# Kernel tuning notes

Measured on AMD Instinct MI355X. Metric: run time of the kernel, lower is better.

Reference implementation:

```python
import jax, jax.numpy as jnp
from jax import lax
import numpy as np

B, T, D, H = 32, 2048, 512, 512


def setup_inputs() -> dict:
    key = jax.random.key(0)
    k1, k2, k3, k4, k5 = jax.random.split(key, 5)
    s = 1.0 / np.sqrt(H)
    return {
        "inputs": jax.random.normal(k1, (B, T, D), dtype=jnp.float32),
        "h_prev": jax.random.normal(k2, (B, H), dtype=jnp.float32),
        # LSTMCell parameters, gate order (i, f, g, o) stacked along first dim
        "W_ih": jax.random.uniform(k3, (4 * H, D), jnp.float32, -s, s),
        "W_hh": jax.random.uniform(k4, (4 * H, H), jnp.float32, -s, s),
        "b": jax.random.uniform(k5, (4 * H,), jnp.float32, -s, s),
    }


def reference(inputs, h_prev, W_ih, W_hh, b):
    # inputs: [B, T, D], h_prev: [B, H]
    batch = inputs.shape[0]
    hid = h_prev.shape[1]
    c_prev = jnp.zeros((batch, hid), dtype=inputs.dtype)
    # Precompute input projections for all timesteps: [T, B, 4H]
    x_proj = jnp.einsum("btd,gd->tbg", inputs, W_ih) + b

    def step(carry, xp_t):
        h, c = carry
        gates = xp_t + h @ W_hh.T  # [B, 4H]
        i, f, g, o = jnp.split(gates, 4, axis=-1)
        i = jax.nn.sigmoid(i)
        f = jax.nn.sigmoid(f)
        g = jnp.tanh(g)
        o = jax.nn.sigmoid(o)
        c_next = f * c + i * g
        h_next = o * jnp.tanh(c_next)
        return (h_next, c_next), None

    (h_last, _), _ = lax.scan(step, (h_prev, c_prev), x_proj)
    return h_last
```

## Files before the change

kernel.cpp:

```cpp
#include <hip/hip_runtime.h>

typedef _Float16 f16;
typedef _Float16 f16x4 __attribute__((ext_vector_type(4)));
typedef _Float16 f16x8 __attribute__((ext_vector_type(8)));
typedef float f32x4 __attribute__((ext_vector_type(4)));
typedef unsigned long long u64;
typedef unsigned short u16;

#define NB 32
#define NT 2048
#define ND 512
#define NH 512
#define NWG 16
#define SENTW 0xFFFFFFFFFFFFFFFFull
#define SENTH ((u16)0xFFFFu)

__device__ __forceinline__ float sigf(float x)  { return 1.0f / (1.0f + __expf(-x)); }
__device__ __forceinline__ float tanhf_(float x){ return 2.0f / (1.0f + __expf(-2.0f * x)) - 1.0f; }

__device__ __forceinline__ bool has_sent(u64 x) {
  u64 a = x & (x >> 8); a &= (a >> 4); a &= (a >> 2); a &= (a >> 1);
  return (a & 0x0001000100010001ull) != 0ull;
}

__device__ __forceinline__ int lds_idx(int w) {
  const int m = w >> 7, c0 = (w & 127) << 2;
  const int kt = c0 >> 5, half = m >> 4;
  const int lane16 = (((c0 & 31) >> 3) << 4) + (m & 15);
  return ((kt * 2 + half) * 64 + lane16) * 8 + (c0 & 7);
}

__global__ void lstm_init(const float* __restrict__ hprev, u64* __restrict__ hg4) {
  const int g = blockIdx.x * 256 + threadIdx.x;
  const int m = g >> 7, c0 = (g & 127) << 2;
  const float* s = hprev + m * NH + c0;
  union { u64 u; f16 h[4]; } pk;
  pk.h[0] = (f16)s[0]; pk.h[1] = (f16)s[1]; pk.h[2] = (f16)s[2]; pk.h[3] = (f16)s[3];
  hg4[g] = pk.u;
  hg4[4096 + g] = SENTW;
  hg4[2 * 4096 + g] = SENTW;
  hg4[3 * 4096 + g] = SENTW;
}

__global__ void __launch_bounds__(256, 1)
lstm_xproj(const float* __restrict__ X, const float* __restrict__ Wih,
           const float* __restrict__ bias, f16* __restrict__ xp) {
  __shared__ f16 x_lds[16384];
  const int tid = threadIdx.x, lane = tid & 63;
  const int wv = tid >> 6, s = wv & 1, bt = wv >> 1;
  const int l15 = lane & 15, ko = (lane >> 4) * 8;
  const int cb = blockIdx.y, tb = blockIdx.x;
  const int colg = cb * 32 + s * 16 + l15;
  const int b0 = bt * 16 + (lane >> 4) * 4;

  f16x8 wf[4][16];
  float bs[4];
#pragma unroll
  for (int q = 0; q < 4; ++q) {
    const size_t grow = (size_t)(q * NH + colg);
    bs[q] = bias[grow];
#pragma unroll
    for (int kt = 0; kt < 16; ++kt) {
      const float* src = Wih + grow * ND + kt * 32 + ko;
      f32x4 u0 = *(const f32x4*)src, u1 = *(const f32x4*)(src + 4);
      f16x8 w;
      w[0]=(f16)u0[0]; w[1]=(f16)u0[1]; w[2]=(f16)u0[2]; w[3]=(f16)u0[3];
      w[4]=(f16)u1[0]; w[5]=(f16)u1[1]; w[6]=(f16)u1[2]; w[7]=(f16)u1[3];
      wf[q][kt] = w;
    }
  }

  for (int tt = 0; tt < 32; ++tt) {
    const int t = tb * 32 + tt;
#pragma unroll
    for (int i = 0; i < 16; ++i) {
      const int w = tid + 256 * i;
      const int m = w >> 7, c0 = (w & 127) << 2;
      f32x4 v = *(const f32x4*)(X + ((size_t)m * NT + t) * ND + c0);
      union { u64 u; f16 h[4]; } pk;
      pk.h[0]=(f16)v[0]; pk.h[1]=(f16)v[1]; pk.h[2]=(f16)v[2]; pk.h[3]=(f16)v[3];
      *(u64*)&x_lds[lds_idx(w)] = pk.u;
    }
    __syncthreads();

    f32x4 acc[4] = {{0,0,0,0},{0,0,0,0},{0,0,0,0},{0,0,0,0}};
#pragma unroll
    for (int kt = 0; kt < 16; ++kt) {
      f16x8 af = *(const f16x8*)&x_lds[((kt * 2 + bt) * 64 + lane) * 8];
      acc[0] = __builtin_amdgcn_mfma_f32_16x16x32_f16(af, wf[0][kt], acc[0], 0, 0, 0);
      acc[1] = __builtin_amdgcn_mfma_f32_16x16x32_f16(af, wf[1][kt], acc[1], 0, 0, 0);
      acc[2] = __builtin_amdgcn_mfma_f32_16x16x32_f16(af, wf[2][kt], acc[2], 0, 0, 0);
      acc[3] = __builtin_amdgcn_mfma_f32_16x16x32_f16(af, wf[3][kt], acc[3], 0, 0, 0);
    }
#pragma unroll
    for (int q = 0; q < 4; ++q) {
      f16x4 o;
      o[0]=(f16)(acc[q][0]+bs[q]); o[1]=(f16)(acc[q][1]+bs[q]);
      o[2]=(f16)(acc[q][2]+bs[q]); o[3]=(f16)(acc[q][3]+bs[q]);
      *(f16x4*)&xp[((((size_t)t * 4 + q) * 512) + colg) * 32 + b0] = o;
    }
    __syncthreads();
  }
}

__global__ void __launch_bounds__(256, 1)
lstm_rec(const float* __restrict__ Whh,
         const f16*   __restrict__ xp,
         float* __restrict__ out,
         u64* __restrict__ hg4) {
  __shared__ f16 h_lin[2][16384];

  const int tid  = threadIdx.x;
  const int wgid = blockIdx.x;
  const int lane = tid & 63;
  const int wv   = tid >> 6, s = wv & 1, bt = wv >> 1;
  const int l15  = lane & 15, ko = (lane >> 4) * 8;
  const int colg = wgid * 32 + s * 16 + l15;
  const int b0   = bt * 16 + (lane >> 4) * 4;

  f16x8 wf[4][16];
#pragma unroll
  for (int q = 0; q < 4; ++q) {
    const size_t grow = (size_t)(q * NH + colg);
#pragma unroll
    for (int kt = 0; kt < 16; ++kt) {
      const float* src = Whh + grow * NH + kt * 32 + ko;
      f32x4 u0 = *(const f32x4*)src, u1 = *(const f32x4*)(src + 4);
      f16x8 w;
      w[0]=(f16)u0[0]; w[1]=(f16)u0[1]; w[2]=(f16)u0[2]; w[3]=(f16)u0[3];
      w[4]=(f16)u1[0]; w[5]=(f16)u1[1]; w[6]=(f16)u1[2]; w[7]=(f16)u1[3];
      wf[q][kt] = w;
    }
  }

  u16* hgh = (u16*)hg4;

  f16x4 xpv[4];
#pragma unroll
  for (int q = 0; q < 4; ++q)
    xpv[q] = *(const f16x4*)&xp[(((size_t)0 * 4 + q) * 512 + colg) * 32 + b0];

  float c[4] = {0.f, 0.f, 0.f, 0.f};

  for (int t = 0; t < NT; ++t) {
    {
      u16* rb = hgh + (size_t)((t + 2) & 3) * 16384;
#pragma unroll
      for (int r = 0; r < 4; ++r)
        __hip_atomic_store(rb + (b0 + r) * 512 + colg, SENTH,
                           __ATOMIC_RELAXED, __HIP_MEMORY_SCOPE_AGENT);
    }
    const int tn = (t < NT - 1) ? t + 1 : NT - 1;
    f16x4 xpn[4];
#pragma unroll
    for (int q = 0; q < 4; ++q)
      xpn[q] = *(const f16x4*)&xp[(((size_t)tn * 4 + q) * 512 + colg) * 32 + b0];

    u64 hv16[16];
    {
      u64* src = hg4 + (size_t)(t & 3) * 4096;
#pragma unroll
      for (int i = 0; i < 16; ++i)
        hv16[i] = __hip_atomic_load(src + tid + 256 * i, __ATOMIC_RELAXED, __HIP_MEMORY_SCOPE_AGENT);
      while (true) {
        unsigned int bad = 0;
#pragma unroll
        for (int i = 0; i < 16; ++i) if (has_sent(hv16[i])) bad |= (1u << i);
        if (!__any(bad != 0)) break;
#pragma unroll
        for (int i = 0; i < 16; ++i)
          if (bad & (1u << i))
            hv16[i] = __hip_atomic_load(src + tid + 256 * i, __ATOMIC_RELAXED, __HIP_MEMORY_SCOPE_AGENT);
      }
    }
    asm volatile("s_waitcnt vmcnt(0)" ::: "memory");

    f16* hb = h_lin[t & 1];
#pragma unroll
    for (int i = 0; i < 16; ++i)
      *(u64*)&hb[lds_idx(tid + 256 * i)] = hv16[i];
    __syncthreads();

    f32x4 acc[4] = {{0,0,0,0},{0,0,0,0},{0,0,0,0},{0,0,0,0}};
#pragma unroll
    for (int kt = 0; kt < 16; ++kt) {
      f16x8 af = *(const f16x8*)&hb[((kt * 2 + bt) * 64 + lane) * 8];
      acc[0] = __builtin_amdgcn_mfma_f32_16x16x32_f16(af, wf[0][kt], acc[0], 0, 0, 0);
      acc[1] = __builtin_amdgcn_mfma_f32_16x16x32_f16(af, wf[1][kt], acc[1], 0, 0, 0);
      acc[2] = __builtin_amdgcn_mfma_f32_16x16x32_f16(af, wf[2][kt], acc[2], 0, 0, 0);
      acc[3] = __builtin_amdgcn_mfma_f32_16x16x32_f16(af, wf[3][kt], acc[3], 0, 0, 0);
    }

    {
      u16* pb = hgh + (size_t)((t + 1) & 3) * 16384;
#pragma unroll
      for (int r = 0; r < 3 + 1; ++r) {
        float gi = acc[0][r] + (float)xpv[0][r];
        float gf = acc[1][r] + (float)xpv[1][r];
        float gg = acc[2][r] + (float)xpv[2][r];
        float go = acc[3][r] + (float)xpv[3][r];
        c[r] = sigf(gf) * c[r] + sigf(gi) * tanhf_(gg);
        float hv = sigf(go) * tanhf_(c[r]);
        union { f16 h; u16 u; } cv; cv.h = (f16)hv;
        __hip_atomic_store(pb + (b0 + r) * 512 + colg, cv.u,
                           __ATOMIC_RELAXED, __HIP_MEMORY_SCOPE_AGENT);
        if (t == NT - 1) out[(size_t)(b0 + r) * NH + colg] = hv;
      }
    }
#pragma unroll
    for (int q = 0; q < 4; ++q) xpv[q] = xpn[q];
  }
}

extern "C" void kernel_launch(void* const* d_in, const int* in_sizes, int n_in,
                              void* d_out, int out_size, void* d_ws, size_t ws_size,
                              hipStream_t stream) {
  const float* X     = (const float*)d_in[0];
  const float* hprev = (const float*)d_in[1];
  const float* Wih   = (const float*)d_in[2];
  const float* Whh   = (const float*)d_in[3];
  const float* bias  = (const float*)d_in[4];
  float* out = (float*)d_out;

  u64* hg4 = (u64*)d_ws;
  f16* xp  = (f16*)((char*)d_ws + (size_t)(1 << 17));

  hipLaunchKernelGGL(lstm_init, dim3(16), dim3(256), 0, stream, hprev, hg4);
  hipLaunchKernelGGL(lstm_xproj, dim3(64, 16), dim3(256), 0, stream, X, Wih, bias, xp);
  hipLaunchKernelGGL(lstm_rec, dim3(NWG), dim3(256), 0, stream, Whh, xp, out, hg4);
}
```

Baseline: 10.04 ms.

## Fuse input projection into recurrent kernel and interleave two batch halves

Drops the separate x-projection GEMM kernel. X is now only converted to fp16, and the recurrent kernel computes W_ih·x on the fly alongside W_hh·h. The batch is split into two independent 16-row halves with separate h exchange buffers, so each workgroup processes one half while the other half's h values propagate between workgroups. The kernel also uses 32 workgroups with a gate-interleaved weight layout, so each lane holds all four gates for one column. This doubles the MFMA work inside the serial recurrence, in exchange for hiding cross-workgroup sync latency and removing the xproj pass.

```diff
diff --git a/kernel.cpp b/kernel.cpp
--- a/kernel.cpp
+++ b/kernel.cpp
@@ -1,7 +1,6 @@
 #include <hip/hip_runtime.h>
 
 typedef _Float16 f16;
-typedef _Float16 f16x4 __attribute__((ext_vector_type(4)));
 typedef _Float16 f16x8 __attribute__((ext_vector_type(8)));
 typedef float f32x4 __attribute__((ext_vector_type(4)));
 typedef unsigned long long u64;
@@ -11,9 +10,10 @@
 #define NT 2048
 #define ND 512
 #define NH 512
-#define NWG 16
-#define SENTW 0xFFFFFFFFFFFFFFFFull
+#define NWG 32
 #define SENTH ((u16)0xFFFFu)
+#define SLOT 8192
+#define SLOT64 2048
 
 __device__ __forceinline__ float sigf(float x)  { return 1.0f / (1.0f + __expf(-x)); }
 __device__ __forceinline__ float tanhf_(float x){ return 2.0f / (1.0f + __expf(-2.0f * x)) - 1.0f; }
@@ -23,192 +23,183 @@
   return (a & 0x0001000100010001ull) != 0ull;
 }
 
-__device__ __forceinline__ int lds_idx(int w) {
-  const int m = w >> 7, c0 = (w & 127) << 2;
-  const int kt = c0 >> 5, half = m >> 4;
-  const int lane16 = (((c0 & 31) >> 3) << 4) + (m & 15);
-  return ((kt * 2 + half) * 64 + lane16) * 8 + (c0 & 7);
-}
-
-__global__ void lstm_init(const float* __restrict__ hprev, u64* __restrict__ hg4) {
+__global__ void lstm_init(const float* __restrict__ hprev, u16* __restrict__ hg) {
   const int g = blockIdx.x * 256 + threadIdx.x;
-  const int m = g >> 7, c0 = (g & 127) << 2;
-  const float* s = hprev + m * NH + c0;
-  union { u64 u; f16 h[4]; } pk;
-  pk.h[0] = (f16)s[0]; pk.h[1] = (f16)s[1]; pk.h[2] = (f16)s[2]; pk.h[3] = (f16)s[3];
-  hg4[g] = pk.u;
-  hg4[4096 + g] = SENTW;
-  hg4[2 * 4096 + g] = SENTW;
-  hg4[3 * 4096 + g] = SENTW;
+  const int ch = g >> 15, r = g & 32767, slot = r >> 13, idx = r & 8191;
+  u16 v;
+  if (slot == 0) {
+    const int m = idx >> 9, col = idx & 511;
+    union { f16 h; u16 u; } cv; cv.h = (f16)hprev[(size_t)(ch * 16 + m) * NH + col];
+    v = cv.u;
+  } else v = SENTH;
+  hg[(size_t)(ch * 4 + slot) * SLOT + idx] = v;
 }
 
 __global__ void __launch_bounds__(256, 1)
-lstm_xproj(const float* __restrict__ X, const float* __restrict__ Wih,
-           const float* __restrict__ bias, f16* __restrict__ xp) {
-  __shared__ f16 x_lds[16384];
-  const int tid = threadIdx.x, lane = tid & 63;
-  const int wv = tid >> 6, s = wv & 1, bt = wv >> 1;
-  const int l15 = lane & 15, ko = (lane >> 4) * 8;
-  const int cb = blockIdx.y, tb = blockIdx.x;
-  const int colg = cb * 32 + s * 16 + l15;
-  const int b0 = bt * 16 + (lane >> 4) * 4;
-
-  f16x8 wf[4][16];
-  float bs[4];
+lstm_xcvt(const float* __restrict__ X, f16* __restrict__ Xh) {
+  const int t = blockIdx.x, ch = blockIdx.y, tid = threadIdx.x;
+  const int b = tid & 15, d0 = (tid >> 4) * 32;
+  const float* src = X + ((size_t)(ch * 16 + b) * NT + t) * ND + d0;
+  f16* dst = Xh + ((size_t)t * 2 + ch) * SLOT;
+  f32x4 v[8];
+#pragma unroll
+  for (int i = 0; i < 8; ++i) v[i] = *(const f32x4*)(src + 4 * i);
 #pragma unroll
   for (int q = 0; q < 4; ++q) {
-    const size_t grow = (size_t)(q * NH + colg);
-    bs[q] = bias[grow];
-#pragma unroll
-    for (int kt = 0; kt < 16; ++kt) {
-      const float* src = Wih + grow * ND + kt * 32 + ko;
-      f32x4 u0 = *(const f32x4*)src, u1 = *(const f32x4*)(src + 4);
-      f16x8 w;
-      w[0]=(f16)u0[0]; w[1]=(f16)u0[1]; w[2]=(f16)u0[2]; w[3]=(f16)u0[3];
-      w[4]=(f16)u1[0]; w[5]=(f16)u1[1]; w[6]=(f16)u1[2]; w[7]=(f16)u1[3];
-      wf[q][kt] = w;
-    }
-  }
-
-  for (int tt = 0; tt < 32; ++tt) {
-    const int t = tb * 32 + tt;
-#pragma unroll
-    for (int i = 0; i < 16; ++i) {
-      const int w = tid + 256 * i;
-      const int m = w >> 7, c0 = (w & 127) << 2;
-      f32x4 v = *(const f32x4*)(X + ((size_t)m * NT + t) * ND + c0);
-      union { u64 u; f16 h[4]; } pk;
-      pk.h[0]=(f16)v[0]; pk.h[1]=(f16)v[1]; pk.h[2]=(f16)v[2]; pk.h[3]=(f16)v[3];
-      *(u64*)&x_lds[lds_idx(w)] = pk.u;
-    }
-    __syncthreads();
-
-    f32x4 acc[4] = {{0,0,0,0},{0,0,0,0},{0,0,0,0},{0,0,0,0}};
-#pragma unroll
-    for (int kt = 0; kt < 16; ++kt) {
-      f16x8 af = *(const f16x8*)&x_lds[((kt * 2 + bt) * 64 + lane) * 8];
-      acc[0] = __builtin_amdgcn_mfma_f32_16x16x32_f16(af, wf[0][kt], acc[0], 0, 0, 0);
-      acc[1] = __builtin_amdgcn_mfma_f32_16x16x32_f16(af, wf[1][kt], acc[1], 0, 0, 0);
-      acc[2] = __builtin_amdgcn_mfma_f32_16x16x32_f16(af, wf[2][kt], acc[2], 0, 0, 0);
-      acc[3] = __builtin_amdgcn_mfma_f32_16x16x32_f16(af, wf[3][kt], acc[3], 0, 0, 0);
-    }
-#pragma unroll
-    for (int q = 0; q < 4; ++q) {
-      f16x4 o;
-      o[0]=(f16)(acc[q][0]+bs[q]); o[1]=(f16)(acc[q][1]+bs[q]);
-      o[2]=(f16)(acc[q][2]+bs[q]); o[3]=(f16)(acc[q][3]+bs[q]);
-      *(f16x4*)&xp[((((size_t)t * 4 + q) * 512) + colg) * 32 + b0] = o;
-    }
-    __syncthreads();
+    f16x8 o;
+#pragma unroll
+    for (int e = 0; e < 8; ++e) o[e] = (f16)v[q * 2 + (e >> 2)][e & 3];
+    *(f16x8*)&dst[((d0 >> 5) * 64 + q * 16 + b) * 8] = o;
   }
 }
 
 __global__ void __launch_bounds__(256, 1)
 lstm_rec(const float* __restrict__ Whh,
-         const f16*   __restrict__ xp,
+         const float* __restrict__ Wih,
+         const float* __restrict__ bias,
+         const f16*   __restrict__ Xh,
          float* __restrict__ out,
-         u64* __restrict__ hg4) {
-  __shared__ f16 h_lin[2][16384];
+         u16*   __restrict__ hg) {
+  __shared__ __align__(16) f16 hA[SLOT];
+  __shared__ __align__(16) f16 hB[SLOT];
 
   const int tid  = threadIdx.x;
   const int wgid = blockIdx.x;
+  const int wv   = tid >> 6;
   const int lane = tid & 63;
-  const int wv   = tid >> 6, s = wv & 1, bt = wv >> 1;
-  const int l15  = lane & 15, ko = (lane >> 4) * 8;
-  const int colg = wgid * 32 + s * 16 + l15;
-  const int b0   = bt * 16 + (lane >> 4) * 4;
-
-  f16x8 wf[4][16];
-#pragma unroll
-  for (int q = 0; q < 4; ++q) {
-    const size_t grow = (size_t)(q * NH + colg);
-#pragma unroll
-    for (int kt = 0; kt < 16; ++kt) {
-      const float* src = Whh + grow * NH + kt * 32 + ko;
-      f32x4 u0 = *(const f32x4*)src, u1 = *(const f32x4*)(src + 4);
-      f16x8 w;
-      w[0]=(f16)u0[0]; w[1]=(f16)u0[1]; w[2]=(f16)u0[2]; w[3]=(f16)u0[3];
-      w[4]=(f16)u1[0]; w[5]=(f16)u1[1]; w[6]=(f16)u1[2]; w[7]=(f16)u1[3];
-      wf[q][kt] = w;
-    }
+  const int l15  = lane & 15;
+  const int lg   = lane >> 4;
+  const int colW = wgid * 16 + wv * 4;
+  const int fq   = l15 & 3, fc = l15 >> 2;
+  const int mycol = colW + lg;
+
+  f16x8 wfh[16], wfx[16];
+#pragma unroll
+  for (int kt = 0; kt < 16; ++kt) {
+    const float* s1 = Whh + ((size_t)fq * NH + colW + fc) * NH + kt * 32 + lg * 8;
+    const float* s2 = Wih + ((size_t)fq * NH + colW + fc) * ND + kt * 32 + lg * 8;
+    f16x8 a, b;
+#pragma unroll
+    for (int e = 0; e < 8; ++e) { a[e] = (f16)s1[e]; b[e] = (f16)s2[e]; }
+    wfh[kt] = a; wfx[kt] = b;
   }
-
-  u16* hgh = (u16*)hg4;
-
-  f16x4 xpv[4];
-#pragma unroll
-  for (int q = 0; q < 4; ++q)
-    xpv[q] = *(const f16x4*)&xp[(((size_t)0 * 4 + q) * 512 + colg) * 32 + b0];
-
-  float c[4] = {0.f, 0.f, 0.f, 0.f};
+  float bs[4];
+#pragma unroll
+  for (int q = 0; q < 4; ++q) bs[q] = bias[q * NH + mycol];
+
+  const int gw0  = l15 * 128 + wv * 32 + lg * 8;
+  const int pidx = l15 * 512 + mycol;
+
+  u64* hg64 = (u64*)hg;
+  float cA = 0.f, cB = 0.f;
+
+  u64 gA[8], gB[8];
+#pragma unroll
+  for (int i = 0; i < 8; ++i)
+    gA[i] = __hip_atomic_load(hg64 + gw0 + i, __ATOMIC_RELAXED, __HIP_MEMORY_SCOPE_AGENT);
+#pragma unroll
+  for (int i = 0; i < 8; ++i)
+    gB[i] = __hip_atomic_load(hg64 + 4 * SLOT64 + gw0 + i, __ATOMIC_RELAXED, __HIP_MEMORY_SCOPE_AGENT);
 
   for (int t = 0; t < NT; ++t) {
     {
-      u16* rb = hgh + (size_t)((t + 2) & 3) * 16384;
-#pragma unroll
-      for (int r = 0; r < 4; ++r)
-        __hip_atomic_store(rb + (b0 + r) * 512 + colg, SENTH,
-                           __ATOMIC_RELAXED, __HIP_MEMORY_SCOPE_AGENT);
-    }
-    const int tn = (t < NT - 1) ? t + 1 : NT - 1;
-    f16x4 xpn[4];
-#pragma unroll
-    for (int q = 0; q < 4; ++q)
-      xpn[q] = *(const f16x4*)&xp[(((size_t)tn * 4 + q) * 512 + colg) * 32 + b0];
-
-    u64 hv16[16];
-    {
-      u64* src = hg4 + (size_t)(t & 3) * 4096;
-#pragma unroll
-      for (int i = 0; i < 16; ++i)
-        hv16[i] = __hip_atomic_load(src + tid + 256 * i, __ATOMIC_RELAXED, __HIP_MEMORY_SCOPE_AGENT);
+      u64* src = hg64 + (size_t)(t & 3) * SLOT64 + gw0;
       while (true) {
-        unsigned int bad = 0;
-#pragma unroll
-        for (int i = 0; i < 16; ++i) if (has_sent(hv16[i])) bad |= (1u << i);
-        if (!__any(bad != 0)) break;
-#pragma unroll
-        for (int i = 0; i < 16; ++i)
+        unsigned bad = 0;
+#pragma unroll
+        for (int i = 0; i < 8; ++i) if (has_sent(gA[i])) bad |= 1u << i;
+        if (!__any(bad)) break;
+#pragma unroll
+        for (int i = 0; i < 8; ++i)
           if (bad & (1u << i))
-            hv16[i] = __hip_atomic_load(src + tid + 256 * i, __ATOMIC_RELAXED, __HIP_MEMORY_SCOPE_AGENT);
-      }
-    }
-    asm volatile("s_waitcnt vmcnt(0)" ::: "memory");
-
-    f16* hb = h_lin[t & 1];
-#pragma unroll
-    for (int i = 0; i < 16; ++i)
-      *(u64*)&hb[lds_idx(tid + 256 * i)] = hv16[i];
+            gA[i] = __hip_atomic_load(src + i, __ATOMIC_RELAXED, __HIP_MEMORY_SCOPE_AGENT);
+      }
+#pragma unroll
+      for (int i = 0; i < 8; ++i)
+        *(u64*)&hA[(((wv * 4 + lg) * 64 + (i >> 1) * 16 + l15) << 3) + 4 * (i & 1)] = gA[i];
+    }
     __syncthreads();
-
-    f32x4 acc[4] = {{0,0,0,0},{0,0,0,0},{0,0,0,0},{0,0,0,0}};
-#pragma unroll
-    for (int kt = 0; kt < 16; ++kt) {
-      f16x8 af = *(const f16x8*)&hb[((kt * 2 + bt) * 64 + lane) * 8];
-      acc[0] = __builtin_amdgcn_mfma_f32_16x16x32_f16(af, wf[0][kt], acc[0], 0, 0, 0);
-      acc[1] = __builtin_amdgcn_mfma_f32_16x16x32_f16(af, wf[1][kt], acc[1], 0, 0, 0);
-      acc[2] = __builtin_amdgcn_mfma_f32_16x16x32_f16(af, wf[2][kt], acc[2], 0, 0, 0);
-      acc[3] = __builtin_amdgcn_mfma_f32_16x16x32_f16(af, wf[3][kt], acc[3], 0, 0, 0);
-    }
-
-    {
-      u16* pb = hgh + (size_t)((t + 1) & 3) * 16384;
-#pragma unroll
-      for (int r = 0; r < 3 + 1; ++r) {
-        float gi = acc[0][r] + (float)xpv[0][r];
-        float gf = acc[1][r] + (float)xpv[1][r];
-        float gg = acc[2][r] + (float)xpv[2][r];
-        float go = acc[3][r] + (float)xpv[3][r];
-        c[r] = sigf(gf) * c[r] + sigf(gi) * tanhf_(gg);
-        float hv = sigf(go) * tanhf_(c[r]);
-        union { f16 h; u16 u; } cv; cv.h = (f16)hv;
-        __hip_atomic_store(pb + (b0 + r) * 512 + colg, cv.u,
-                           __ATOMIC_RELAXED, __HIP_MEMORY_SCOPE_AGENT);
-        if (t == NT - 1) out[(size_t)(b0 + r) * NH + colg] = hv;
-      }
-    }
-#pragma unroll
-    for (int q = 0; q < 4; ++q) xpv[q] = xpn[q];
+    {
+      const f16* xb = Xh + ((size_t)t * 2 + 0) * SLOT + lane * 8;
+      f32x4 acc = {0, 0, 0, 0};
+#pragma unroll
+      for (int kt = 0; kt < 16; ++kt) {
+        f16x8 hf = *(const f16x8*)&hA[(kt * 64 + lane) * 8];
+        acc = __builtin_amdgcn_mfma_f32_16x16x32_f16(wfh[kt], hf, acc, 0, 0, 0);
+      }
+#pragma unroll
+      for (int kt = 0; kt < 16; ++kt) {
+        f16x8 xf = *(const f16x8*)(xb + kt * 512);
+        acc = __builtin_amdgcn_mfma_f32_16x16x32_f16(wfx[kt], xf, acc, 0, 0, 0);
+      }
+      float ig = sigf(acc[0] + bs[0]);
+      float fg = sigf(acc[1] + bs[1]);
+      float gg = tanhf_(acc[2] + bs[2]);
+      float og = sigf(acc[3] + bs[3]);
+      cA = fg * cA + ig * gg;
+      float hv = og * tanhf_(cA);
+      union { f16 h; u16 u; } cv; cv.h = (f16)hv;
+      __hip_atomic_store(hg + (size_t)((t + 1) & 3) * SLOT + pidx, cv.u,
+                         __ATOMIC_RELAXED, __HIP_MEMORY_SCOPE_AGENT);
+      __hip_atomic_store(hg + (size_t)((t + 3) & 3) * SLOT + pidx, SENTH,
+                         __ATOMIC_RELAXED, __HIP_MEMORY_SCOPE_AGENT);
+      if (t == NT - 1) out[(size_t)l15 * NH + mycol] = hv;
+      if (t < NT - 1) {
+        u64* nsrc = hg64 + (size_t)((t + 1) & 3) * SLOT64 + gw0;
+#pragma unroll
+        for (int i = 0; i < 8; ++i)
+          gA[i] = __hip_atomic_load(nsrc + i, __ATOMIC_RELAXED, __HIP_MEMORY_SCOPE_AGENT);
+      }
+    }
+    {
+      u64* src = hg64 + (size_t)(4 + (t & 3)) * SLOT64 + gw0;
+      while (true) {
+        unsigned bad = 0;
+#pragma unroll
+        for (int i = 0; i < 8; ++i) if (has_sent(gB[i])) bad |= 1u << i;
+        if (!__any(bad)) break;
+#pragma unroll
+        for (int i = 0; i < 8; ++i)
+          if (bad & (1u << i))
+            gB[i] = __hip_atomic_load(src + i, __ATOMIC_RELAXED, __HIP_MEMORY_SCOPE_AGENT);
+      }
+#pragma unroll
+      for (int i = 0; i < 8; ++i)
+        *(u64*)&hB[(((wv * 4 + lg) * 64 + (i >> 1) * 16 + l15) << 3) + 4 * (i & 1)] = gB[i];
+    }
+    __syncthreads();
+    {
+      const f16* xb = Xh + ((size_t)t * 2 + 1) * SLOT + lane * 8;
+      f32x4 acc = {0, 0, 0, 0};
+#pragma unroll
+      for (int kt = 0; kt < 16; ++kt) {
+        f16x8 hf = *(const f16x8*)&hB[(kt * 64 + lane) * 8];
+        acc = __builtin_amdgcn_mfma_f32_16x16x32_f16(wfh[kt], hf, acc, 0, 0, 0);
+      }
+#pragma unroll
+      for (int kt = 0; kt < 16; ++kt) {
+        f16x8 xf = *(const f16x8*)(xb + kt * 512);
+        acc = __builtin_amdgcn_mfma_f32_16x16x32_f16(wfx[kt], xf, acc, 0, 0, 0);
+      }
+      float ig = sigf(acc[0] + bs[0]);
+      float fg = sigf(acc[1] + bs[1]);
+      float gg = tanhf_(acc[2] + bs[2]);
+      float og = sigf(acc[3] + bs[3]);
+      cB = fg * cB + ig * gg;
+      float hv = og * tanhf_(cB);
+      union { f16 h; u16 u; } cv; cv.h = (f16)hv;
+      __hip_atomic_store(hg + (size_t)(4 + ((t + 1) & 3)) * SLOT + pidx, cv.u,
+                         __ATOMIC_RELAXED, __HIP_MEMORY_SCOPE_AGENT);
+      __hip_atomic_store(hg + (size_t)(4 + ((t + 3) & 3)) * SLOT + pidx, SENTH,
+                         __ATOMIC_RELAXED, __HIP_MEMORY_SCOPE_AGENT);
+      if (t == NT - 1) out[(size_t)(16 + l15) * NH + mycol] = hv;
+      if (t < NT - 1) {
+        u64* nsrc = hg64 + (size_t)(4 + ((t + 1) & 3)) * SLOT64 + gw0;
+#pragma unroll
+        for (int i = 0; i < 8; ++i)
+          gB[i] = __hip_atomic_load(nsrc + i, __ATOMIC_RELAXED, __HIP_MEMORY_SCOPE_AGENT);
+      }
+    }
   }
 }
 
@@ -222,10 +213,11 @@
   const float* bias  = (const float*)d_in[4];
   float* out = (float*)d_out;
 
-  u64* hg4 = (u64*)d_ws;
-  f16* xp  = (f16*)((char*)d_ws + (size_t)(1 << 17));
-
-  hipLaunchKernelGGL(lstm_init, dim3(16), dim3(256), 0, stream, hprev, hg4);
-  hipLaunchKernelGGL(lstm_xproj, dim3(64, 16), dim3(256), 0, stream, X, Wih, bias, xp);
-  hipLaunchKernelGGL(lstm_rec, dim3(NWG), dim3(256), 0, stream, Whh, xp, out, hg4);
-}
+  u16* hg = (u16*)d_ws;
+  f16* Xh = (f16*)((char*)d_ws + (size_t)(1 << 17));
+
+  hipLaunchKernelGGL(lstm_init, dim3(256), dim3(256), 0, stream, hprev, hg);
+  hipLaunchKernelGGL(lstm_xcvt, dim3(NT, 2), dim3(256), 0, stream, X, Xh);
+  hipLaunchKernelGGL(lstm_rec, dim3(NWG), dim3(256), 0, stream,
+                     Whh, Wih, bias, Xh, out, hg);
+}
```

After: 23.29 ms. 2.32x slower.

## Interleave gate rows in MFMA tiles so each lane owns all four gates

Applied to the files above, without the earlier changes.

The W_hh and W_ih fragments are re-laid out so that each 16-row MFMA tile interleaves the i,f,g,o gate rows of four hidden columns. Each lane's accumulator then holds all four gates for one (batch, column) pair, and the x-projection can be stored as one packed u64 per element. The h gather is changed to contiguous per-thread loads, and the x-projection grid is widened to 128x32 blocks with fewer weights held per block. The intent is to cut the per-step load count and address math on the serial recurrence path, at the cost of a new layout that has to match exactly across all three kernels.

```diff
diff --git a/kernel.cpp b/kernel.cpp
--- a/kernel.cpp
+++ b/kernel.cpp
@@ -1,13 +1,12 @@
 #include <hip/hip_runtime.h>
 
 typedef _Float16 f16;
-typedef _Float16 f16x4 __attribute__((ext_vector_type(4)));
 typedef _Float16 f16x8 __attribute__((ext_vector_type(8)));
 typedef float f32x4 __attribute__((ext_vector_type(4)));
 typedef unsigned long long u64;
 typedef unsigned short u16;
-
-#define NB 32
+typedef unsigned int u32;
+
 #define NT 2048
 #define ND 512
 #define NH 512
@@ -23,192 +22,205 @@
   return (a & 0x0001000100010001ull) != 0ull;
 }
 
-__device__ __forceinline__ int lds_idx(int w) {
-  const int m = w >> 7, c0 = (w & 127) << 2;
-  const int kt = c0 >> 5, half = m >> 4;
-  const int lane16 = (((c0 & 31) >> 3) << 4) + (m & 15);
-  return ((kt * 2 + half) * 64 + lane16) * 8 + (c0 & 7);
-}
-
-__global__ void lstm_init(const float* __restrict__ hprev, u64* __restrict__ hg4) {
+__device__ __forceinline__ int frag_idx(int b, int k0) {
+  return ((k0 >> 5) * 2 + (b >> 4)) * 64 + ((k0 & 31) >> 3) * 16 + (b & 15);
+}
+
+__global__ void lstm_init(const float* __restrict__ hprev, u64* __restrict__ hg) {
   const int g = blockIdx.x * 256 + threadIdx.x;
-  const int m = g >> 7, c0 = (g & 127) << 2;
-  const float* s = hprev + m * NH + c0;
-  union { u64 u; f16 h[4]; } pk;
-  pk.h[0] = (f16)s[0]; pk.h[1] = (f16)s[1]; pk.h[2] = (f16)s[2]; pk.h[3] = (f16)s[3];
-  hg4[g] = pk.u;
-  hg4[4096 + g] = SENTW;
-  hg4[2 * 4096 + g] = SENTW;
-  hg4[3 * 4096 + g] = SENTW;
+  const int slot = g >> 12, idx = g & 4095;
+  u64 v = SENTW;
+  if (slot == 0) {
+    const int b = idx >> 7, c0 = (idx & 127) << 2;
+    const float* s = hprev + b * NH + c0;
+    union { u64 u; f16 h[4]; } pk;
+    pk.h[0] = (f16)s[0]; pk.h[1] = (f16)s[1]; pk.h[2] = (f16)s[2]; pk.h[3] = (f16)s[3];
+    v = pk.u;
+  }
+  __hip_atomic_store(hg + g, v, __ATOMIC_RELAXED, __HIP_MEMORY_SCOPE_AGENT);
 }
 
 __global__ void __launch_bounds__(256, 1)
 lstm_xproj(const float* __restrict__ X, const float* __restrict__ Wih,
-           const float* __restrict__ bias, f16* __restrict__ xp) {
-  __shared__ f16 x_lds[16384];
+           const float* __restrict__ bias, u64* __restrict__ xp) {
+  __shared__ __align__(16) f16 x_lds[16384];
   const int tid = threadIdx.x, lane = tid & 63;
-  const int wv = tid >> 6, s = wv & 1, bt = wv >> 1;
-  const int l15 = lane & 15, ko = (lane >> 4) * 8;
-  const int cb = blockIdx.y, tb = blockIdx.x;
-  const int colg = cb * 32 + s * 16 + l15;
-  const int b0 = bt * 16 + (lane >> 4) * 4;
-
-  f16x8 wf[4][16];
+  const int wv = tid >> 6, l15 = lane & 15, lg = lane >> 4;
+  const int tb = blockIdx.x, cb = blockIdx.y;
+  const int colbase = cb * 16 + wv * 4;
+
+  f16x8 wf[16];
+#pragma unroll
+  for (int kt = 0; kt < 16; ++kt) {
+    const float* src = Wih + ((size_t)(l15 & 3) * NH + colbase + (l15 >> 2)) * ND + kt * 32 + lg * 8;
+    f32x4 u0 = *(const f32x4*)src, u1 = *(const f32x4*)(src + 4);
+    f16x8 w;
+    w[0]=(f16)u0[0]; w[1]=(f16)u0[1]; w[2]=(f16)u0[2]; w[3]=(f16)u0[3];
+    w[4]=(f16)u1[0]; w[5]=(f16)u1[1]; w[6]=(f16)u1[2]; w[7]=(f16)u1[3];
+    wf[kt] = w;
+  }
+  const int mycol = colbase + lg;
   float bs[4];
 #pragma unroll
-  for (int q = 0; q < 4; ++q) {
-    const size_t grow = (size_t)(q * NH + colg);
-    bs[q] = bias[grow];
+  for (int q = 0; q < 4; ++q) bs[q] = bias[q * NH + mycol];
+
+  const int gb = tid >> 3, gc0 = (tid & 7) * 64;
+
+  for (int tt = 0; tt < 16; ++tt) {
+    const int t = tb * 16 + tt;
+    const float* xs = X + ((size_t)gb * NT + t) * ND + gc0;
+#pragma unroll
+    for (int i = 0; i < 8; ++i) {
+      f32x4 v0 = *(const f32x4*)(xs + 8 * i);
+      f32x4 v1 = *(const f32x4*)(xs + 8 * i + 4);
+      f16x8 h8;
+      h8[0]=(f16)v0[0]; h8[1]=(f16)v0[1]; h8[2]=(f16)v0[2]; h8[3]=(f16)v0[3];
+      h8[4]=(f16)v1[0]; h8[5]=(f16)v1[1]; h8[6]=(f16)v1[2]; h8[7]=(f16)v1[3];
+      *(f16x8*)&x_lds[frag_idx(gb, gc0 + 8 * i) * 8] = h8;
+    }
+    __syncthreads();
+
+    f32x4 acc0 = {0,0,0,0}, acc1 = {0,0,0,0};
 #pragma unroll
     for (int kt = 0; kt < 16; ++kt) {
-      const float* src = Wih + grow * ND + kt * 32 + ko;
+      f16x8 b0 = *(const f16x8*)&x_lds[((kt * 2 + 0) * 64 + lane) * 8];
+      f16x8 b1 = *(const f16x8*)&x_lds[((kt * 2 + 1) * 64 + lane) * 8];
+      acc0 = __builtin_amdgcn_mfma_f32_16x16x32_f16(wf[kt], b0, acc0, 0, 0, 0);
+      acc1 = __builtin_amdgcn_mfma_f32_16x16x32_f16(wf[kt], b1, acc1, 0, 0, 0);
+    }
+#pragma unroll
+    for (int bh = 0; bh < 2; ++bh) {
+      const f32x4& a = bh ? acc1 : acc0;
+      union { u64 u; f16 h[4]; } pk;
+      pk.h[0] = (f16)(a[0] + bs[0]); pk.h[1] = (f16)(a[1] + bs[1]);
+      pk.h[2] = (f16)(a[2] + bs[2]); pk.h[3] = (f16)(a[3] + bs[3]);
+      __hip_atomic_store(xp + ((size_t)t * NH + mycol) * 32 + bh * 16 + l15, pk.u,
+                         __ATOMIC_RELAXED, __HIP_MEMORY_SCOPE_AGENT);
+    }
+    __syncthreads();
+  }
+}
+
+__global__ void __launch_bounds__(256, 1)
+lstm_rec(const float* __restrict__ Whh,
+         const u64*   __restrict__ xp,
+         float* __restrict__ out,
+         u64*   __restrict__ hg) {
+  __shared__ __align__(16) f16 hbuf[2][16384];
+
+  const int tid = threadIdx.x, lane = tid & 63;
+  const int wv = tid >> 6, l15 = lane & 15, lg = lane >> 4;
+  const int wgid = blockIdx.x;
+  const int colW = wgid * 32 + wv * 8;
+
+  f16x8 wfa[2][16];
+#pragma unroll
+  for (int a = 0; a < 2; ++a)
+#pragma unroll
+    for (int kt = 0; kt < 16; ++kt) {
+      const float* src = Whh + ((size_t)(l15 & 3) * NH + colW + a * 4 + (l15 >> 2)) * NH + kt * 32 + lg * 8;
       f32x4 u0 = *(const f32x4*)src, u1 = *(const f32x4*)(src + 4);
       f16x8 w;
       w[0]=(f16)u0[0]; w[1]=(f16)u0[1]; w[2]=(f16)u0[2]; w[3]=(f16)u0[3];
       w[4]=(f16)u1[0]; w[5]=(f16)u1[1]; w[6]=(f16)u1[2]; w[7]=(f16)u1[3];
-      wf[q][kt] = w;
-    }
-  }
-
-  for (int tt = 0; tt < 32; ++tt) {
-    const int t = tb * 32 + tt;
-#pragma unroll
-    for (int i = 0; i < 16; ++i) {
-      const int w = tid + 256 * i;
-      const int m = w >> 7, c0 = (w & 127) << 2;
-      f32x4 v = *(const f32x4*)(X + ((size_t)m * NT + t) * ND + c0);
-      union { u64 u; f16 h[4]; } pk;
-      pk.h[0]=(f16)v[0]; pk.h[1]=(f16)v[1]; pk.h[2]=(f16)v[2]; pk.h[3]=(f16)v[3];
-      *(u64*)&x_lds[lds_idx(w)] = pk.u;
-    }
-    __syncthreads();
-
-    f32x4 acc[4] = {{0,0,0,0},{0,0,0,0},{0,0,0,0},{0,0,0,0}};
-#pragma unroll
-    for (int kt = 0; kt < 16; ++kt) {
-      f16x8 af = *(const f16x8*)&x_lds[((kt * 2 + bt) * 64 + lane) * 8];
-      acc[0] = __builtin_amdgcn_mfma_f32_16x16x32_f16(af, wf[0][kt], acc[0], 0, 0, 0);
-      acc[1] = __builtin_amdgcn_mfma_f32_16x16x32_f16(af, wf[1][kt], acc[1], 0, 0, 0);
-      acc[2] = __builtin_amdgcn_mfma_f32_16x16x32_f16(af, wf[2][kt], acc[2], 0, 0, 0);
-      acc[3] = __builtin_amdgcn_mfma_f32_16x16x32_f16(af, wf[3][kt], acc[3], 0, 0, 0);
-    }
-#pragma unroll
-    for (int q = 0; q < 4; ++q) {
-      f16x4 o;
-      o[0]=(f16)(acc[q][0]+bs[q]); o[1]=(f16)(acc[q][1]+bs[q]);
-      o[2]=(f16)(acc[q][2]+bs[q]); o[3]=(f16)(acc[q][3]+bs[q]);
-      *(f16x4*)&xp[((((size_t)t * 4 + q) * 512) + colg) * 32 + b0] = o;
-    }
-    __syncthreads();
-  }
-}
-
-__global__ void __launch_bounds__(256, 1)
-lstm_rec(const float* __restrict__ Whh,
-         const f16*   __restrict__ xp,
-         float* __restrict__ out,
-         u64* __restrict__ hg4) {
-  __shared__ f16 h_lin[2][16384];
-
-  const int tid  = threadIdx.x;
-  const int wgid = blockIdx.x;
-  const int lane = tid & 63;
-  const int wv   = tid >> 6, s = wv & 1, bt = wv >> 1;
-  const int l15  = lane & 15, ko = (lane >> 4) * 8;
-  const int colg = wgid * 32 + s * 16 + l15;
-  const int b0   = bt * 16 + (lane >> 4) * 4;
-
-  f16x8 wf[4][16];
-#pragma unroll
-  for (int q = 0; q < 4; ++q) {
-    const size_t grow = (size_t)(q * NH + colg);
-#pragma unroll
-    for (int kt = 0; kt < 16; ++kt) {
-      const float* src = Whh + grow * NH + kt * 32 + ko;
-      f32x4 u0 = *(const f32x4*)src, u1 = *(const f32x4*)(src + 4);
-      f16x8 w;
-      w[0]=(f16)u0[0]; w[1]=(f16)u0[1]; w[2]=(f16)u0[2]; w[3]=(f16)u0[3];
-      w[4]=(f16)u1[0]; w[5]=(f16)u1[1]; w[6]=(f16)u1[2]; w[7]=(f16)u1[3];
-      wf[q][kt] = w;
-    }
-  }
-
-  u16* hgh = (u16*)hg4;
-
-  f16x4 xpv[4];
-#pragma unroll
-  for (int q = 0; q < 4; ++q)
-    xpv[q] = *(const f16x4*)&xp[(((size_t)0 * 4 + q) * 512 + colg) * 32 + b0];
-
-  float c[4] = {0.f, 0.f, 0.f, 0.f};
+      wfa[a][kt] = w;
+    }
+
+  const int gb = tid & 31, gc0 = (tid >> 5) * 64;
+  const int gword = gb * 128 + (tid >> 5) * 16;
+
+  u16* hgh = (u16*)hg;
+  int paddr[2][2], qaddr[2][2];
+#pragma unroll
+  for (int a = 0; a < 2; ++a)
+#pragma unroll
+    for (int bh = 0; bh < 2; ++bh) {
+      const int b = bh * 16 + l15, col = colW + a * 4 + lg;
+      paddr[a][bh] = b * NH + col;
+      qaddr[a][bh] = col * 32 + b;
+    }
+
+  float c[2][2] = {{0.f, 0.f}, {0.f, 0.f}};
 
   for (int t = 0; t < NT; ++t) {
-    {
-      u16* rb = hgh + (size_t)((t + 2) & 3) * 16384;
-#pragma unroll
-      for (int r = 0; r < 4; ++r)
-        __hip_atomic_store(rb + (b0 + r) * 512 + colg, SENTH,
-                           __ATOMIC_RELAXED, __HIP_MEMORY_SCOPE_AGENT);
-    }
-    const int tn = (t < NT - 1) ? t + 1 : NT - 1;
-    f16x4 xpn[4];
-#pragma unroll
-    for (int q = 0; q < 4; ++q)
-      xpn[q] = *(const f16x4*)&xp[(((size_t)tn * 4 + q) * 512 + colg) * 32 + b0];
-
-    u64 hv16[16];
-    {
-      u64* src = hg4 + (size_t)(t & 3) * 4096;
+    const u64* xpt = xp + (size_t)t * 16384;
+    u64 xv[2][2];
+#pragma unroll
+    for (int a = 0; a < 2; ++a)
+#pragma unroll
+      for (int bh = 0; bh < 2; ++bh) xv[a][bh] = xpt[qaddr[a][bh]];
+
+    {
+      u16* rb = hgh + ((size_t)((t + 2) & 3) << 14);
+#pragma unroll
+      for (int a = 0; a < 2; ++a)
+#pragma unroll
+        for (int bh = 0; bh < 2; ++bh)
+          __hip_atomic_store(rb + paddr[a][bh], SENTH, __ATOMIC_RELAXED, __HIP_MEMORY_SCOPE_AGENT);
+    }
+
+    u64 g[16];
+    {
+      const u64* src = hg + ((size_t)(t & 3) << 12) + gword;
 #pragma unroll
       for (int i = 0; i < 16; ++i)
-        hv16[i] = __hip_atomic_load(src + tid + 256 * i, __ATOMIC_RELAXED, __HIP_MEMORY_SCOPE_AGENT);
+        g[i] = __hip_atomic_load(src + i, __ATOMIC_RELAXED, __HIP_MEMORY_SCOPE_AGENT);
       while (true) {
-        unsigned int bad = 0;
-#pragma unroll
-        for (int i = 0; i < 16; ++i) if (has_sent(hv16[i])) bad |= (1u << i);
+        u32 bad = 0;
+#pragma unroll
+        for (int i = 0; i < 16; ++i) if (has_sent(g[i])) bad |= 1u << i;
         if (!__any(bad != 0)) break;
 #pragma unroll
         for (int i = 0; i < 16; ++i)
           if (bad & (1u << i))
-            hv16[i] = __hip_atomic_load(src + tid + 256 * i, __ATOMIC_RELAXED, __HIP_MEMORY_SCOPE_AGENT);
+            g[i] = __hip_atomic_load(src + i, __ATOMIC_RELAXED, __HIP_MEMORY_SCOPE_AGENT);
       }
     }
     asm volatile("s_waitcnt vmcnt(0)" ::: "memory");
 
-    f16* hb = h_lin[t & 1];
-#pragma unroll
-    for (int i = 0; i < 16; ++i)
-      *(u64*)&hb[lds_idx(tid + 256 * i)] = hv16[i];
+    {
+      u64* hb64 = (u64*)hbuf[t & 1];
+#pragma unroll
+      for (int i = 0; i < 16; i += 2) {
+        const int fi = frag_idx(gb, gc0 + i * 4) * 2;
+        hb64[fi] = g[i];
+        hb64[fi + 1] = g[i + 1];
+      }
+    }
     __syncthreads();
 
-    f32x4 acc[4] = {{0,0,0,0},{0,0,0,0},{0,0,0,0},{0,0,0,0}};
-#pragma unroll
-    for (int kt = 0; kt < 16; ++kt) {
-      f16x8 af = *(const f16x8*)&hb[((kt * 2 + bt) * 64 + lane) * 8];
-      acc[0] = __builtin_amdgcn_mfma_f32_16x16x32_f16(af, wf[0][kt], acc[0], 0, 0, 0);
-      acc[1] = __builtin_amdgcn_mfma_f32_16x16x32_f16(af, wf[1][kt], acc[1], 0, 0, 0);
-      acc[2] = __builtin_amdgcn_mfma_f32_16x16x32_f16(af, wf[2][kt], acc[2], 0, 0, 0);
-      acc[3] = __builtin_amdgcn_mfma_f32_16x16x32_f16(af, wf[3][kt], acc[3], 0, 0, 0);
-    }
-
-    {
-      u16* pb = hgh + (size_t)((t + 1) & 3) * 16384;
-#pragma unroll
-      for (int r = 0; r < 3 + 1; ++r) {
-        float gi = acc[0][r] + (float)xpv[0][r];
-        float gf = acc[1][r] + (float)xpv[1][r];
-        float gg = acc[2][r] + (float)xpv[2][r];
-        float go = acc[3][r] + (float)xpv[3][r];
-        c[r] = sigf(gf) * c[r] + sigf(gi) * tanhf_(gg);
-        float hv = sigf(go) * tanhf_(c[r]);
-        union { f16 h; u16 u; } cv; cv.h = (f16)hv;
-        __hip_atomic_store(pb + (b0 + r) * 512 + colg, cv.u,
-                           __ATOMIC_RELAXED, __HIP_MEMORY_SCOPE_AGENT);
-        if (t == NT - 1) out[(size_t)(b0 + r) * NH + colg] = hv;
+    f32x4 acc[2][2] = {{{0,0,0,0},{0,0,0,0}},{{0,0,0,0},{0,0,0,0}}};
+    {
+      const f16* hb = hbuf[t & 1];
+#pragma unroll
+      for (int kt = 0; kt < 16; ++kt) {
+        f16x8 b0 = *(const f16x8*)&hb[((kt * 2 + 0) * 64 + lane) * 8];
+        f16x8 b1 = *(const f16x8*)&hb[((kt * 2 + 1) * 64 + lane) * 8];
+        acc[0][0] = __builtin_amdgcn_mfma_f32_16x16x32_f16(wfa[0][kt], b0, acc[0][0], 0, 0, 0);
+        acc[1][0] = __builtin_amdgcn_mfma_f32_16x16x32_f16(wfa[1][kt], b0, acc[1][0], 0, 0, 0);
+        acc[0][1] = __builtin_amdgcn_mfma_f32_16x16x32_f16(wfa[0][kt], b1, acc[0][1], 0, 0, 0);
+        acc[1][1] = __builtin_amdgcn_mfma_f32_16x16x32_f16(wfa[1][kt], b1, acc[1][1], 0, 0, 0);
       }
     }
-#pragma unroll
-    for (int q = 0; q < 4; ++q) xpv[q] = xpn[q];
+
+    {
+      u16* pb = hgh + ((size_t)((t + 1) & 3) << 14);
+#pragma unroll
+      for (int a = 0; a < 2; ++a)
+#pragma unroll
+        for (int bh = 0; bh < 2; ++bh) {
+          const f16* xg = (const f16*)&xv[a][bh];
+          float gi = acc[a][bh][0] + (float)xg[0];
+          float gf = acc[a][bh][1] + (float)xg[1];
+          float gg = acc[a][bh][2] + (float)xg[2];
+          float go = acc[a][bh][3] + (float)xg[3];
+          c[a][bh] = sigf(gf) * c[a][bh] + sigf(gi) * tanhf_(gg);
+          float hv = sigf(go) * tanhf_(c[a][bh]);
+          union { f16 h; u16 u; } cv; cv.h = (f16)hv;
+          __hip_atomic_store(pb + paddr[a][bh], cv.u, __ATOMIC_RELAXED, __HIP_MEMORY_SCOPE_AGENT);
+          if (t == NT - 1) out[paddr[a][bh]] = hv;
+        }
+    }
   }
 }
 
@@ -222,10 +234,10 @@
   const float* bias  = (const float*)d_in[4];
   float* out = (float*)d_out;
 
-  u64* hg4 = (u64*)d_ws;
-  f16* xp  = (f16*)((char*)d_ws + (size_t)(1 << 17));
-
-  hipLaunchKernelGGL(lstm_init, dim3(16), dim3(256), 0, stream, hprev, hg4);
-  hipLaunchKernelGGL(lstm_xproj, dim3(64, 16), dim3(256), 0, stream, X, Wih, bias, xp);
-  hipLaunchKernelGGL(lstm_rec, dim3(NWG), dim3(256), 0, stream, Whh, xp, out, hg4);
-}
+  u64* hg = (u64*)d_ws;
+  u64* xp = (u64*)((char*)d_ws + (size_t)(1 << 17));
+
+  hipLaunchKernelGGL(lstm_init, dim3(64), dim3(256), 0, stream, hprev, hg);
+  hipLaunchKernelGGL(lstm_xproj, dim3(128, 32), dim3(256), 0, stream, X, Wih, bias, xp);
+  hipLaunchKernelGGL(lstm_rec, dim3(NWG), dim3(256), 0, stream, Whh, xp, out, hg);
+}
```

Measured after the change: 12.58 ms. +25.3%, slower.
